# Kernel tuning notes

Hardware: AMD Instinct MI355X
Metric: run time of the kernel (lower is better)

Reference implementation:

```python
import jax, jax.numpy as jnp
import numpy as np

N_NODES = 50000
N_EDGES = 600000
CLASSIC_DIM = 128
GRAPH_OUTPUT_DIM = 96
NUM_RELATIONS = 4


def setup_inputs() -> dict:
    key = jax.random.key(0)
    ks = jax.random.split(key, 10)
    x = jax.random.normal(ks[0], (N_NODES, CLASSIC_DIM), dtype=jnp.float32)
    edge_index = jax.random.randint(ks[1], (2, N_EDGES), 0, N_NODES, dtype=jnp.int64)
    edge_type = jax.random.randint(ks[2], (N_EDGES,), 0, NUM_RELATIONS, dtype=jnp.int64)
    s1 = 1.0 / np.sqrt(CLASSIC_DIM)
    W_root1 = jax.random.normal(ks[3], (CLASSIC_DIM, CLASSIC_DIM), dtype=jnp.float32) * s1
    W_rel1 = jax.random.normal(ks[4], (NUM_RELATIONS, CLASSIC_DIM, CLASSIC_DIM), dtype=jnp.float32) * s1
    b1 = jnp.zeros((CLASSIC_DIM,), dtype=jnp.float32)
    W_root2 = jax.random.normal(ks[5], (CLASSIC_DIM, GRAPH_OUTPUT_DIM), dtype=jnp.float32) * s1
    W_rel2 = jax.random.normal(ks[6], (NUM_RELATIONS, CLASSIC_DIM, GRAPH_OUTPUT_DIM), dtype=jnp.float32) * s1
    b2 = jnp.zeros((GRAPH_OUTPUT_DIM,), dtype=jnp.float32)
    return {"classic_features": x, "edge_index": edge_index, "edge_type": edge_type,
            "W_root1": W_root1, "W_rel1": W_rel1, "b1": b1,
            "W_root2": W_root2, "W_rel2": W_rel2, "b2": b2}


def _rgcn_layer(x, edge_index, edge_type, W_root, W_rel, b):
    # RGCN: h_i = W_root x_i + b + sum_r (1/deg_{i,r}) * W_r * sum_{j in N_r(i)} x_j
    # Aggregate-then-transform (valid by linearity) to keep the matmul small.
    src, dst = edge_index[0], edge_index[1]
    msgs = x[src]  # [E, d_in] irregular gather
    out = x @ W_root + b
    n = x.shape[0]
    num_rel = W_rel.shape[0]
    for r in range(num_rel):  # small fixed loop over relation types
        mask = (edge_type == r).astype(x.dtype)  # [E]
        agg = jax.ops.segment_sum(msgs * mask[:, None], dst, num_segments=n)  # [N, d_in]
        deg = jax.ops.segment_sum(mask, dst, num_segments=n)  # [N]
        agg = agg / jnp.maximum(deg, 1.0)[:, None]  # mean per relation (PyG default norm)
        out = out + agg @ W_rel[r]
    return out


def reference(classic_features, edge_index, edge_type, W_root1, W_rel1, b1, W_root2, W_rel2, b2):
    h = _rgcn_layer(classic_features, edge_index, edge_type, W_root1, W_rel1, b1)
    h = jax.nn.relu(h)
    # dropout(0.2) is identity in eval mode
    out = _rgcn_layer(h, edge_index, edge_type, W_root2, W_rel2, b2)
    return out
```

## Files before the change

### kernel.cpp

```cpp
#include <hip/hip_runtime.h>

#define DIM_IN 128
#define NREL 4
#define KTOT (DIM_IN + NREL * DIM_IN)
#define CAP 32
#define SLOTS 30

typedef __attribute__((ext_vector_type(8))) short short8;
typedef __attribute__((ext_vector_type(4))) float floatx4;

__device__ inline unsigned short f2bf(float f) {
    union { float f; unsigned int i; } c;
    c.f = f;
    unsigned int r = c.i + 0x7FFF + ((c.i >> 16) & 1);
    return (unsigned short)(r >> 16);
}
__device__ inline float bf2f(unsigned short u) {
    union { unsigned int i; float f; } c;
    c.i = ((unsigned int)u) << 16;
    return c.f;
}

__device__ inline void gload16_lds(const void* g, void* l) {
    __builtin_amdgcn_global_load_lds((const __attribute__((address_space(1))) unsigned int*)g,
                                     (__attribute__((address_space(3))) unsigned int*)l,
                                     16, 0, 0);
}

__global__ __launch_bounds__(256) void prep_kernel(
    const float* __restrict__ x, unsigned short* __restrict__ xb, int n4,
    const float* __restrict__ Wroot1, const float* __restrict__ Wrel1,
    unsigned short* __restrict__ Wt1,
    const float* __restrict__ Wroot2, const float* __restrict__ Wrel2,
    unsigned short* __restrict__ Wt2,
    const int* __restrict__ ei, const int* __restrict__ et,
    unsigned short* __restrict__ bucket, int E) {
    int t = blockIdx.x * 256 + threadIdx.x;
    if (t < E) {
        int b = ei[E + t] * NREL + et[t];
        unsigned short* line = bucket + (size_t)b * CAP;
        int slot = atomicAdd((int*)line, 1);
        if (slot < SLOTS) line[2 + slot] = (unsigned short)ei[t];
    }
    if (t < n4) {
        float4 v = ((const float4*)x)[t];
        ushort4 o;
        o.x = f2bf(v.x); o.y = f2bf(v.y); o.z = f2bf(v.z); o.w = f2bf(v.w);
        ((ushort4*)xb)[t] = o;
    }
    if (t < 128 * KTOT) {
        int n = t / KTOT, k = t - n * KTOT;
        float v = (k < DIM_IN) ? Wroot1[(size_t)k * 128 + n]
                               : Wrel1[(size_t)(k - DIM_IN) * 128 + n];
        Wt1[t] = f2bf(v);
    }
    if (t < 96 * KTOT) {
        int n = t / KTOT, k = t - n * KTOT;
        float v = (k < DIM_IN) ? Wroot2[(size_t)k * 96 + n]
                               : Wrel2[(size_t)(k - DIM_IN) * 96 + n];
        Wt2[t] = f2bf(v);
    }
}

__global__ __launch_bounds__(256) void agg_kernel(
    const unsigned short* __restrict__ feat, const unsigned short* __restrict__ bucket,
    unsigned short* __restrict__ agg, int nb) {
    int l16 = threadIdx.x & 15;
    int g = (blockIdx.x * 256 + threadIdx.x) >> 4;
    if (g >= nb) return;
    const unsigned short* bk = bucket + (size_t)g * CAP;
    unsigned int wv = ((const unsigned int*)bk)[l16];
    int cnt = __shfl((int)wv, 0, 16);
    int m = (cnt < SLOTS) ? cnt : SLOTS;
    const unsigned short* fb = feat + l16 * 8;
    float acc[8];
#pragma unroll
    for (int j = 0; j < 8; j++) acc[j] = 0.f;
    for (int base = 0; base < m; base += 16) {
        int mm = m - base;
        if (mm > 16) mm = 16;
        int pick = (l16 < mm) ? l16 : (mm - 1);
        int e = base + pick;
        unsigned int word = (unsigned int)__shfl((int)wv, 1 + (e >> 1), 16);
        int idx = (int)((word >> (16 * (e & 1))) & 0xFFFFu);
        int s0 = __shfl(idx, 0, 16);
        short8 u = *(const short8*)(fb + (size_t)s0 * DIM_IN);
        for (int j = 1; j < mm; j++) {
            int sn = __shfl(idx, j, 16);
            short8 un = *(const short8*)(fb + (size_t)sn * DIM_IN);
#pragma unroll
            for (int c = 0; c < 8; c++) acc[c] += bf2f((unsigned short)u[c]);
            u = un;
        }
#pragma unroll
        for (int c = 0; c < 8; c++) acc[c] += bf2f((unsigned short)u[c]);
    }
    float sc = (cnt > 0) ? (1.0f / (float)cnt) : 0.f;
    short8 o;
#pragma unroll
    for (int j = 0; j < 8; j++) o[j] = (short)f2bf(acc[j] * sc);
    *(short8*)(agg + (size_t)g * DIM_IN + l16 * 8) = o;
}

template <int NOUT, bool STORE_BF16_RELU>
__global__ __launch_bounds__(256) void mfma_gemm_kernel(
    const unsigned short* __restrict__ xb,
    const unsigned short* __restrict__ agg,
    const unsigned short* __restrict__ Wt,
    const float* __restrict__ bias,
    void* __restrict__ outp,
    int N) {
    constexpr int NT = NOUT / 32;
    constexpr int APAN = 64 * 32;
    constexpr int BPAN = NOUT * 32;
    constexpr int KS = KTOT / 64;
    __shared__ unsigned short sA[2][2 * APAN];
    __shared__ unsigned short sB[2][2 * BPAN];
    const int t = threadIdx.x;
    const int w = t >> 6;
    const int lane = t & 63;
    const int q = lane >> 4;
    const int l15 = lane & 15;
    const int wm = w >> 1, wn = w & 1;
    const int m0 = blockIdx.x * 64;

    floatx4 acc[2][NT];
#pragma unroll
    for (int mt = 0; mt < 2; mt++)
#pragma unroll
        for (int nt = 0; nt < NT; nt++) acc[mt][nt] = (floatx4)0.f;

    auto stageA = [&](int ks, int buf) {
        const int k0 = ks * 64;
#pragma unroll
        for (int r = 0; r < 2; r++) {
            int idx = t + r * 256;
            int panel = idx >> 8;
            int rem = idx & 255;
            int row = rem >> 2, ch = rem & 3;
            int qq = ch ^ ((row >> 1) & 3);
            int rowg = m0 + row;
            if (rowg >= N) rowg = N - 1;
            int col = panel * 32 + qq * 8;
            const unsigned short* gp =
                (k0 < DIM_IN)
                    ? (xb + (size_t)rowg * DIM_IN + k0 + col)
                    : (agg + (size_t)rowg * (NREL * DIM_IN) + (k0 - DIM_IN) + col);
            gload16_lds(gp, &sA[buf][(size_t)idx * 8]);
        }
    };
    auto stageB = [&](int ks, int buf) {
        const int k0 = ks * 64;
#pragma unroll
        for (int r = 0; r < (NOUT * 8) / 256; r++) {
            int idx = t + r * 256;
            int panel = idx / (NOUT * 4);
            int rem = idx - panel * (NOUT * 4);
            int nrow = rem >> 2, ch = rem & 3;
            int qq = ch ^ ((nrow >> 1) & 3);
            gload16_lds(Wt + (size_t)nrow * KTOT + k0 + panel * 32 + qq * 8,
                        &sB[buf][(size_t)idx * 8]);
        }
    };

    const int qsw = q ^ ((l15 >> 1) & 3);

    stageA(0, 0);
    stageB(0, 0);
    __syncthreads();
    for (int ks = 0; ks < KS; ks++) {
        const int cur = ks & 1;
        if (ks + 1 < KS) {
            stageA(ks + 1, cur ^ 1);
            stageB(ks + 1, cur ^ 1);
        }
#pragma unroll
        for (int s = 0; s < 2; s++) {
            short8 aF[2], bF[NT];
#pragma unroll
            for (int mt = 0; mt < 2; mt++)
                aF[mt] = *(const short8*)(&sA[cur][(size_t)s * APAN +
                                                   (size_t)(wm * 32 + mt * 16 + l15) * 32 + qsw * 8]);
#pragma unroll
            for (int nt = 0; nt < NT; nt++)
                bF[nt] = *(const short8*)(&sB[cur][(size_t)s * BPAN +
                                                   (size_t)(wn * (NOUT / 2) + nt * 16 + l15) * 32 + qsw * 8]);
#pragma unroll
            for (int mt = 0; mt < 2; mt++)
#pragma unroll
                for (int nt = 0; nt < NT; nt++)
                    acc[mt][nt] = __builtin_amdgcn_mfma_f32_16x16x32_bf16(aF[mt], bF[nt],
                                                                          acc[mt][nt], 0, 0, 0);
        }
        __syncthreads();
    }

#pragma unroll
    for (int nt = 0; nt < NT; nt++) {
        int colg = wn * (NOUT / 2) + nt * 16 + l15;
        float bv = bias[colg];
#pragma unroll
        for (int mt = 0; mt < 2; mt++) {
            int rbase = m0 + wm * 32 + mt * 16 + q * 4;
#pragma unroll
            for (int r = 0; r < 4; r++) {
                int grow = rbase + r;
                if (grow < N) {
                    float v = acc[mt][nt][r] + bv;
                    if (STORE_BF16_RELU) {
                        v = fmaxf(v, 0.f);
                        ((unsigned short*)outp)[(size_t)grow * NOUT + colg] = f2bf(v);
                    } else {
                        ((float*)outp)[(size_t)grow * NOUT + colg] = v;
                    }
                }
            }
        }
    }
}

extern "C" void kernel_launch(void* const* d_in, const int* in_sizes, int n_in,
                              void* d_out, int out_size, void* d_ws, size_t ws_size,
                              hipStream_t stream) {
    const float* x = (const float*)d_in[0];
    const int* ei = (const int*)d_in[1];
    const int* et = (const int*)d_in[2];
    const float* Wroot1 = (const float*)d_in[3];
    const float* Wrel1 = (const float*)d_in[4];
    const float* b1 = (const float*)d_in[5];
    const float* Wroot2 = (const float*)d_in[6];
    const float* Wrel2 = (const float*)d_in[7];
    const float* b2 = (const float*)d_in[8];
    float* out = (float*)d_out;

    int N = in_sizes[0] / DIM_IN;
    int E = in_sizes[2];
    int nb = N * NREL;

    char* p = (char*)d_ws;
    unsigned short* xb = (unsigned short*)p;     p += (size_t)N * DIM_IN * 2;
    unsigned short* hb = (unsigned short*)p;     p += (size_t)N * DIM_IN * 2;
    unsigned short* agg = (unsigned short*)p;    p += (size_t)nb * DIM_IN * 2;
    unsigned short* Wt1 = (unsigned short*)p;    p += (size_t)128 * KTOT * 2;
    unsigned short* Wt2 = (unsigned short*)p;    p += (size_t)96 * KTOT * 2;
    unsigned short* bucket = (unsigned short*)p; p += (size_t)nb * CAP * 2;
    if ((size_t)(p - (char*)d_ws) > ws_size) return;

    int n4 = N * DIM_IN / 4;
    int prepWork = n4;
    if (prepWork < E) prepWork = E;
    if (prepWork < 128 * KTOT) prepWork = 128 * KTOT;

    hipMemsetAsync(bucket, 0, (size_t)nb * CAP * 2, stream);
    prep_kernel<<<(prepWork + 255) / 256, 256, 0, stream>>>(
        x, xb, n4, Wroot1, Wrel1, Wt1, Wroot2, Wrel2, Wt2, ei, et, bucket, E);

    int gAgg = (nb * 16 + 255) / 256;
    int gB = (N + 63) / 64;
    agg_kernel<<<gAgg, 256, 0, stream>>>(xb, bucket, agg, nb);
    mfma_gemm_kernel<128, true><<<gB, 256, 0, stream>>>(xb, agg, Wt1, b1, hb, N);
    agg_kernel<<<gAgg, 256, 0, stream>>>(hb, bucket, agg, nb);
    mfma_gemm_kernel<96, false><<<gB, 256, 0, stream>>>(hb, agg, Wt2, b2, out, N);
}
```

Baseline: 235.8 us.

## Batch gather loads in aggregation and enlarge GEMM tile to 128 rows

The aggregation kernel now issues up to eight independent neighbor-row loads into a register array before accumulating. Before, each load was chained one step ahead of the add, so this adds memory-level parallelism. The GEMM block tile grows from 64 to 128 rows, with each wave owning 32 rows across the full output width. This halves the block count and reuses each staged weight panel across more rows. The cost is more registers and LDS per block, which could lower occupancy.

```diff
diff --git a/kernel.cpp b/kernel.cpp
--- a/kernel.cpp
+++ b/kernel.cpp
@@ -76,24 +76,26 @@
     float acc[8];
 #pragma unroll
     for (int j = 0; j < 8; j++) acc[j] = 0.f;
-    for (int base = 0; base < m; base += 16) {
+    for (int base = 0; base < m; base += 8) {
         int mm = m - base;
-        if (mm > 16) mm = 16;
-        int pick = (l16 < mm) ? l16 : (mm - 1);
-        int e = base + pick;
-        unsigned int word = (unsigned int)__shfl((int)wv, 1 + (e >> 1), 16);
-        int idx = (int)((word >> (16 * (e & 1))) & 0xFFFFu);
-        int s0 = __shfl(idx, 0, 16);
-        short8 u = *(const short8*)(fb + (size_t)s0 * DIM_IN);
-        for (int j = 1; j < mm; j++) {
-            int sn = __shfl(idx, j, 16);
-            short8 un = *(const short8*)(fb + (size_t)sn * DIM_IN);
-#pragma unroll
-            for (int c = 0; c < 8; c++) acc[c] += bf2f((unsigned short)u[c]);
-            u = un;
-        }
-#pragma unroll
-        for (int c = 0; c < 8; c++) acc[c] += bf2f((unsigned short)u[c]);
+        if (mm > 8) mm = 8;
+        short8 u[8];
+#pragma unroll
+        for (int j = 0; j < 8; j++) {
+            if (j < mm) {
+                int e = base + j;
+                unsigned int word = (unsigned int)__shfl((int)wv, 1 + (e >> 1), 16);
+                int idx = (int)((word >> (16 * (e & 1))) & 0xFFFFu);
+                u[j] = *(const short8*)(fb + (size_t)idx * DIM_IN);
+            }
+        }
+#pragma unroll
+        for (int j = 0; j < 8; j++) {
+            if (j < mm) {
+#pragma unroll
+                for (int c = 0; c < 8; c++) acc[c] += bf2f((unsigned short)u[j][c]);
+            }
+        }
     }
     float sc = (cnt > 0) ? (1.0f / (float)cnt) : 0.f;
     short8 o;
@@ -110,8 +112,9 @@
     const float* __restrict__ bias,
     void* __restrict__ outp,
     int N) {
-    constexpr int NT = NOUT / 32;
-    constexpr int APAN = 64 * 32;
+    constexpr int BM = 128;
+    constexpr int NT = NOUT / 16;
+    constexpr int APAN = BM * 32;
     constexpr int BPAN = NOUT * 32;
     constexpr int KS = KTOT / 64;
     __shared__ unsigned short sA[2][2 * APAN];
@@ -121,8 +124,7 @@
     const int lane = t & 63;
     const int q = lane >> 4;
     const int l15 = lane & 15;
-    const int wm = w >> 1, wn = w & 1;
-    const int m0 = blockIdx.x * 64;
+    const int m0 = blockIdx.x * BM;
 
     floatx4 acc[2][NT];
 #pragma unroll
@@ -133,10 +135,10 @@
     auto stageA = [&](int ks, int buf) {
         const int k0 = ks * 64;
 #pragma unroll
-        for (int r = 0; r < 2; r++) {
+        for (int r = 0; r < 4; r++) {
             int idx = t + r * 256;
-            int panel = idx >> 8;
-            int rem = idx & 255;
+            int panel = idx >> 9;
+            int rem = idx & 511;
             int row = rem >> 2, ch = rem & 3;
             int qq = ch ^ ((row >> 1) & 3);
             int rowg = m0 + row;
@@ -180,11 +182,11 @@
 #pragma unroll
             for (int mt = 0; mt < 2; mt++)
                 aF[mt] = *(const short8*)(&sA[cur][(size_t)s * APAN +
-                                                   (size_t)(wm * 32 + mt * 16 + l15) * 32 + qsw * 8]);
+                                                   (size_t)(w * 32 + mt * 16 + l15) * 32 + qsw * 8]);
 #pragma unroll
             for (int nt = 0; nt < NT; nt++)
                 bF[nt] = *(const short8*)(&sB[cur][(size_t)s * BPAN +
-                                                   (size_t)(wn * (NOUT / 2) + nt * 16 + l15) * 32 + qsw * 8]);
+                                                   (size_t)(nt * 16 + l15) * 32 + qsw * 8]);
 #pragma unroll
             for (int mt = 0; mt < 2; mt++)
 #pragma unroll
@@ -197,11 +199,11 @@
 
 #pragma unroll
     for (int nt = 0; nt < NT; nt++) {
-        int colg = wn * (NOUT / 2) + nt * 16 + l15;
+        int colg = nt * 16 + l15;
         float bv = bias[colg];
 #pragma unroll
         for (int mt = 0; mt < 2; mt++) {
-            int rbase = m0 + wm * 32 + mt * 16 + q * 4;
+            int rbase = m0 + w * 32 + mt * 16 + q * 4;
 #pragma unroll
             for (int r = 0; r < 4; r++) {
                 int grow = rbase + r;
@@ -256,7 +258,7 @@
         x, xb, n4, Wroot1, Wrel1, Wt1, Wroot2, Wrel2, Wt2, ei, et, bucket, E);
 
     int gAgg = (nb * 16 + 255) / 256;
-    int gB = (N + 63) / 64;
+    int gB = (N + 127) / 128;
     agg_kernel<<<gAgg, 256, 0, stream>>>(xb, bucket, agg, nb);
     mfma_gemm_kernel<128, true><<<gB, 256, 0, stream>>>(xb, agg, Wt1, b1, hb, N);
     agg_kernel<<<gAgg, 256, 0, stream>>>(hb, bucket, agg, nb);
```

After: 237.0 us. About the same (+0.5%).
